# Kernel tuning notes

Measured on AMD Instinct MI355X. Metric: run time of the kernel, lower is better.

## Reference

```python
import jax, jax.numpy as jnp
import numpy as np

WIN = 7          # window height/width
P = 10           # prompts_len
HEADS = 12
B0 = 32          # image batch (spa_prompts batch)
NW = 64          # windows per image
NW_TOK = WIN * WIN  # 49


def _relative_position_index(w):
    coords = np.stack(np.meshgrid(np.arange(w), np.arange(w), indexing='ij'))  # [2,w,w]
    flat = coords.reshape(2, -1)                        # [2, w*w]
    rel = flat[:, :, None] - flat[:, None, :]           # [2, w*w, w*w]
    rel = rel.transpose(1, 2, 0).astype(np.int64)       # [w*w, w*w, 2]
    rel[..., 0] += w - 1
    rel[..., 1] += w - 1
    rel[..., 0] *= 2 * w - 1
    return rel.sum(-1)                                  # [w*w, w*w]

REL_IDX = jnp.asarray(_relative_position_index(WIN))    # [49,49] int


def setup_inputs() -> dict:
    key = jax.random.key(0)
    ks = jax.random.split(key, 8)
    dim = 384
    return {
        'x': jax.random.normal(ks[0], (B0 * NW, NW_TOK, dim), jnp.float32),
        'spa_prompts': jax.random.normal(ks[1], (B0, P, dim), jnp.float32),
        'mask': jax.random.normal(ks[2], (NW, NW_TOK, NW_TOK), jnp.float32),
        'bias_table': jax.random.normal(ks[3], (169, HEADS), jnp.float32) * 0.02,
        'w_qkv': jax.random.normal(ks[4], (3 * dim, dim), jnp.float32) * 0.02,
        'b_qkv': jax.random.normal(ks[5], (3 * dim,), jnp.float32) * 0.02,
        'w_proj': jax.random.normal(ks[6], (dim, dim), jnp.float32) * 0.02,
        'b_proj': jax.random.normal(ks[7], (dim,), jnp.float32) * 0.02,
    }


def reference(x, spa_prompts, mask, bias_table, w_qkv, b_qkv, w_proj, b_proj):
    B_, Nw, C = x.shape
    b0 = spa_prompts.shape[0]
    nW = B_ // b0
    hd = C // HEADS
    scale = hd ** -0.5

    # broadcast prompts to every window and prepend
    prompts = jnp.broadcast_to(spa_prompts[:, None], (b0, nW, P, C)).reshape(B_, P, C)
    xc = jnp.concatenate([prompts, x], axis=1)          # [B_, N, C], N = P + Nw
    N = xc.shape[1]

    qkv = xc @ w_qkv.T + b_qkv                          # [B_, N, 3C]
    qkv = qkv.reshape(B_, N, 3, HEADS, hd).transpose(2, 0, 3, 1, 4)
    q, k, v = qkv[0], qkv[1], qkv[2]                    # [B_, H, N, hd]

    attn_weight = jnp.einsum('bhnd,bhmd->bhnm', q, k)   # unscaled, returned

    # relative position bias gathered for the window block, padded over prompt rows/cols
    rpb = bias_table[REL_IDX.reshape(-1)].reshape(NW_TOK, NW_TOK, HEADS)
    rpb = rpb.transpose(2, 0, 1)                        # [H, 49, 49]
    bias_full = jnp.pad(rpb, ((0, 0), (P, 0), (P, 0)))  # [H, N, N]

    attn = attn_weight * scale + bias_full[None]

    mask_full = jnp.pad(mask, ((0, 0), (P, 0), (P, 0)))  # [nW, N, N]
    attn = attn.reshape(b0, nW, HEADS, N, N) + mask_full[None, :, None]
    attn = jax.nn.softmax(attn.reshape(B_, HEADS, N, N), axis=-1)

    out = jnp.einsum('bhnm,bhmd->bnhd', attn, v).reshape(B_, N, C)
    out = out @ w_proj.T + b_proj

    prompts_out = out[:, :P].reshape(b0, nW, P, C).mean(axis=1)
    x_out = out[:, P:]
    return (x_out, attn_weight, prompts_out)
```

## Files before the change

### kernel.cpp

```cpp
#include <hip/hip_runtime.h>
#include <hip/hip_bf16.h>

#define P     10
#define NTOK  59
#define HEADS 12
#define NWTOK 49

#define AW_OFF 38535168
#define PO_OFF 124096512

typedef __attribute__((ext_vector_type(8))) short short8;
typedef __attribute__((ext_vector_type(8))) unsigned short ushort8;
typedef __attribute__((ext_vector_type(4))) float floatx4;
typedef float f4u __attribute__((ext_vector_type(4), aligned(4)));
typedef unsigned int uint_g __attribute__((address_space(1)));
typedef unsigned int uint_l __attribute__((address_space(3)));

__device__ __forceinline__ unsigned short f2b(float f) {
  unsigned u = __builtin_bit_cast(unsigned, f);
  u += 0x7fffu + ((u >> 16) & 1u);
  return (unsigned short)(u >> 16);
}

__device__ __forceinline__ void gll16(const void* g, void* l) {
  __builtin_amdgcn_global_load_lds((const uint_g*)g, (uint_l*)l, 16, 0, 0);
}

__device__ __forceinline__ int xcd_swz(int bid, int nwg) {
  const int q = nwg >> 3, r = nwg & 7;
  const int xcd = bid & 7, ord = bid >> 3;
  return (xcd < r ? xcd * (q + 1) : r * (q + 1) + (xcd - r) * q) + ord;
}

__global__ __launch_bounds__(256) void convert_w_kernel(
    const float* __restrict__ w, unsigned short* __restrict__ wb) {
  const int i = (blockIdx.x * 256 + threadIdx.x) * 8;
  const float4 a = *(const float4*)(w + i);
  const float4 b = *(const float4*)(w + i + 4);
  ushort8 o;
  o[0] = f2b(a.x); o[1] = f2b(a.y); o[2] = f2b(a.z); o[3] = f2b(a.w);
  o[4] = f2b(b.x); o[5] = f2b(b.y); o[6] = f2b(b.z); o[7] = f2b(b.w);
  *(ushort8*)(wb + i) = o;
}

__global__ __launch_bounds__(256) void combo_kernel(
    const float* __restrict__ mask, const float* __restrict__ bias_table,
    float* __restrict__ combo) {
  const int bid = blockIdx.x;
  const int h = bid % HEADS, wnd = bid / HEADS;
#pragma unroll
  for (int e0 = 0; e0 < 4096; e0 += 256) {
    const int e = e0 + threadIdx.x;
    const int ti = e >> 6, tj = e & 63;
    float v = 0.f;
    if (ti >= P && ti < NTOK && tj >= P && tj < NTOK) {
      const int a = ti - P, c = tj - P;
      const int ai = a / 7, aj = a - ai * 7;
      const int bi = c / 7, bj = c - bi * 7;
      const int ridx = (ai - bi + 6) * 13 + (aj - bj + 6);
      v = bias_table[ridx * HEADS + h] + mask[((size_t)wnd * 49 + a) * 49 + c];
    }
    combo[((size_t)bid << 12) + e] = v;
  }
}

__global__ __launch_bounds__(256) void gemm_qkv_kernel(
    const unsigned short* __restrict__ xb, const unsigned short* __restrict__ xp,
    const unsigned short* __restrict__ Bw, const float* __restrict__ b_qkv,
    unsigned short* __restrict__ qkx, unsigned short* __restrict__ qkp) {
  __shared__ unsigned short sbuf[18432];
  unsigned short* Asw = sbuf;
  unsigned short* Bsw = sbuf + 8192;
  const int t = threadIdx.x;
  const int w = t >> 6, lane = t & 63;
  const int lr = lane & 15, lg = lane >> 4;
  const int w0 = w >> 1, w1 = w & 1;
  const int wg = xcd_swz(blockIdx.x, 9 * 787);
  const int cb = wg % 9;
  const int my = wg / 9;
  const bool isP = my >= 784;
  const int n0 = cb * 128;
  const int srow = lane >> 3, cpos = lane & 7;

  floatx4 acc[4][4];
#pragma unroll
  for (int mr = 0; mr < 4; ++mr)
#pragma unroll
    for (int nc = 0; nc < 4; ++nc) acc[mr][nc] = (floatx4)0.f;

  for (int k0 = 0; k0 < 384; k0 += 64) {
#pragma unroll
    for (int i = 0; i < 4; ++i) {
      const int r = (w * 4 + i) * 8 + srow;
      const int c = cpos ^ (r & 7);
      const unsigned short* asrc;
      if (!isP) {
        asrc = xb + (size_t)(my * 128 + r) * 384 + k0 + c * 8;
      } else {
        int mp = (my - 784) * 128 + r;
        if (mp > 319) mp = 319;
        asrc = xp + (size_t)mp * 384 + k0 + c * 8;
      }
      gll16(asrc, Asw + (w * 4 + i) * 512);
      gll16(Bw + (size_t)(n0 + r) * 384 + k0 + c * 8, Bsw + (w * 4 + i) * 512);
    }
    __syncthreads();
#pragma unroll
    for (int kh = 0; kh < 2; ++kh) {
      short8 af[4], bf[4];
#pragma unroll
      for (int mr = 0; mr < 4; ++mr) {
        const int r = w0 * 64 + mr * 16 + lr;
        af[mr] = *(const short8*)(Asw + r * 64 + (((kh * 4 + lg) ^ (r & 7)) * 8));
      }
#pragma unroll
      for (int nc = 0; nc < 4; ++nc) {
        const int r = w1 * 64 + nc * 16 + lr;
        bf[nc] = *(const short8*)(Bsw + r * 64 + (((kh * 4 + lg) ^ (r & 7)) * 8));
      }
#pragma unroll
      for (int mr = 0; mr < 4; ++mr)
#pragma unroll
        for (int nc = 0; nc < 4; ++nc)
          acc[mr][nc] = __builtin_amdgcn_mfma_f32_16x16x32_bf16(
              af[mr], bf[nc], acc[mr][nc], 0, 0, 0);
    }
    __syncthreads();
  }

  const int sec = cb / 3;
  const int nis = (cb - sec * 3) * 128;
  float bias[4];
#pragma unroll
  for (int nc = 0; nc < 4; ++nc)
    bias[nc] = b_qkv[n0 + w1 * 64 + nc * 16 + lr];

  unsigned short* rp = sbuf + w * 4608;
#pragma unroll
  for (int mr = 0; mr < 4; ++mr)
#pragma unroll
    for (int nc = 0; nc < 4; ++nc)
#pragma unroll
      for (int reg = 0; reg < 4; ++reg)
        rp[(mr * 16 + lg * 4 + reg) * 72 + nc * 16 + lr] =
            f2b(acc[mr][nc][reg] + bias[nc]);
  __syncthreads();

  const int rr = lane;
  unsigned short* dst = nullptr;
  if (!isP) {
    const int m = my * 128 + w0 * 64 + rr;
    const int bb = m / 49, tok = m - bb * 49;
    dst = qkx + ((size_t)(bb * 3 + sec) * 49 + tok) * 384 + nis + w1 * 64;
  } else {
    const int mp = (my - 784) * 128 + w0 * 64 + rr;
    if (mp < 320) {
      const int b0 = mp / 10, ptok = mp - b0 * 10;
      dst = qkp + ((size_t)(b0 * 3 + sec) * 10 + ptok) * 384 + nis + w1 * 64;
    }
  }
  if (dst) {
#pragma unroll
    for (int u = 0; u < 8; ++u)
      *(ushort8*)(dst + u * 8) = *(const ushort8*)(rp + rr * 72 + u * 8);
  }
}

__global__ __launch_bounds__(256) void attn_proj_kernel(
    const unsigned short* __restrict__ qkx, const unsigned short* __restrict__ qkp,
    const float* __restrict__ combo, const unsigned short* __restrict__ wproj,
    const float* __restrict__ b_proj, float* __restrict__ aw_out,
    float* __restrict__ x_out, float* __restrict__ pbuf) {
  __shared__ char lds[74752];
  unsigned short* Obuf = (unsigned short*)lds;
  unsigned short* qs   = (unsigned short*)(lds + 50176);
  unsigned short* ks   = (unsigned short*)(lds + 55296);
  unsigned short* vt   = (unsigned short*)(lds + 60416);
  unsigned short* Bst  = (unsigned short*)(lds + 50176);

  const int b = blockIdx.x;
  const int t = threadIdx.x;
  const int w = t >> 6, lane = t & 63, lr = lane & 15, lg = lane >> 4;
  const float scale = 0.17677669529663687f;
  const int q = w * 16 + lr;

  ushort8 nq, nk, nv;
  const int srow_ = t >> 2, sdc = (t & 3) * 8;
  auto load_head = [&](int h) {
    if (t < 236) {
      if (srow_ < P) {
        const unsigned short* pb =
            qkp + ((size_t)((b >> 6) * 3) * 10 + srow_) * 384 + h * 32 + sdc;
        nq = *(const ushort8*)(pb);
        nk = *(const ushort8*)(pb + 10 * 384);
        nv = *(const ushort8*)(pb + 20 * 384);
      } else {
        const unsigned short* xbp =
            qkx + ((size_t)(b * 3) * 49 + (srow_ - P)) * 384 + h * 32 + sdc;
        nq = *(const ushort8*)(xbp);
        nk = *(const ushort8*)(xbp + 49 * 384);
        nv = *(const ushort8*)(xbp + 98 * 384);
      }
    }
  };

  if (t < 160) vt[(t / 5) * 74 + 59 + (t % 5)] = 0;
  load_head(0);

  for (int h = 0; h < HEADS; ++h) {
    __syncthreads();
    if (t < 236) {
      *(ushort8*)(qs + srow_ * 40 + sdc) = nq;
      *(ushort8*)(ks + srow_ * 40 + sdc) = nk;
#pragma unroll
      for (int j = 0; j < 8; ++j) vt[(sdc + j) * 74 + srow_] = nv[j];
    }
    if (h + 1 < HEADS) load_head(h + 1);
    __syncthreads();

    const short8 qa = *(const short8*)(qs + q * 40 + lg * 8);
    floatx4 sacc[4];
#pragma unroll
    for (int nt = 0; nt < 4; ++nt) {
      const short8 kb = *(const short8*)(ks + (nt * 16 + lr) * 40 + lg * 8);
      sacc[nt] =
          __builtin_amdgcn_mfma_f32_16x16x32_bf16(kb, qa, (floatx4)0.f, 0, 0, 0);
    }

    if (q < NTOK) {
      float* rowp = aw_out + ((size_t)(b * HEADS + h)) * 3481 + q * 59;
#pragma unroll
      for (int nt = 0; nt < 3; ++nt)
        *(f4u*)(rowp + nt * 16 + lg * 4) = __builtin_bit_cast(f4u, sacc[nt]);
      if (lg < 2) {
        *(f4u*)(rowp + 48 + lg * 4) = __builtin_bit_cast(f4u, sacc[3]);
      } else if (lg == 2) {
        rowp[56] = sacc[3][0]; rowp[57] = sacc[3][1]; rowp[58] = sacc[3][2];
      }
    }

    const float* comb =
        combo + (((size_t)((b & 63) * HEADS + h)) << 12) + q * 64;
    float ev[4][4];
    float mx = -3.0e38f;
#pragma unroll
    for (int nt = 0; nt < 4; ++nt) {
      const float4 c4 = *(const float4*)(comb + nt * 16 + lg * 4);
      const float cc[4] = {c4.x, c4.y, c4.z, c4.w};
#pragma unroll
      for (int reg = 0; reg < 4; ++reg) {
        const int kk2 = nt * 16 + lg * 4 + reg;
        const float v = (q < NTOK && kk2 < NTOK)
                            ? fmaf(sacc[nt][reg], scale, cc[reg])
                            : -3.0e38f;
        ev[nt][reg] = v;
        mx = fmaxf(mx, v);
      }
    }
    mx = fmaxf(mx, __shfl_xor(mx, 16));
    mx = fmaxf(mx, __shfl_xor(mx, 32));
    float sm = 0.f;
#pragma unroll
    for (int nt = 0; nt < 4; ++nt)
#pragma unroll
      for (int reg = 0; reg < 4; ++reg) {
        const float e = __expf(ev[nt][reg] - mx);
        ev[nt][reg] = e;
        sm += e;
      }
    sm += __shfl_xor(sm, 16);
    sm += __shfl_xor(sm, 32);
    const float inv = 1.0f / sm;

    unsigned pk[4][2];
#pragma unroll
    for (int nt = 0; nt < 4; ++nt)
#pragma unroll
      for (int pp = 0; pp < 2; ++pp)
        pk[nt][pp] = (unsigned)f2b(ev[nt][2 * pp] * inv) |
                     ((unsigned)f2b(ev[nt][2 * pp + 1] * inv) << 16);

    floatx4 oacc[2];
    oacc[0] = (floatx4)0.f; oacc[1] = (floatx4)0.f;
#pragma unroll
    for (int kk = 0; kk < 2; ++kk) {
      unsigned W4[4];
#pragma unroll
      for (int jp = 0; jp < 4; ++jp) {
        const int srcl = lr + 16 * (2 * (lg & 1) + (jp >> 1));
        const int lo = __shfl((int)pk[2 * kk][jp & 1], srcl);
        const int hi = __shfl((int)pk[2 * kk + 1][jp & 1], srcl);
        W4[jp] = (lg >> 1) ? (unsigned)hi : (unsigned)lo;
      }
      uint4 wu; wu.x = W4[0]; wu.y = W4[1]; wu.z = W4[2]; wu.w = W4[3];
      const short8 pa = __builtin_bit_cast(short8, wu);
#pragma unroll
      for (int nt = 0; nt < 2; ++nt) {
        const short8 vb =
            *(const short8*)(vt + (nt * 16 + lr) * 74 + kk * 32 + lg * 8);
        oacc[nt] =
            __builtin_amdgcn_mfma_f32_16x16x32_bf16(pa, vb, oacc[nt], 0, 0, 0);
      }
    }

#pragma unroll
    for (int nt = 0; nt < 2; ++nt)
#pragma unroll
      for (int reg = 0; reg < 4; ++reg)
        Obuf[(w * 16 + lg * 4 + reg) * 392 + h * 32 + nt * 16 + lr] =
            f2b(oacc[nt][reg]);
  }

  ushort8 bst[6];
  auto load_proj = [&](int s) {
    const int nh_ = s / 6, kch_ = s % 6;
#pragma unroll
    for (int i = 0; i < 6; ++i) {
      const int g = w * 6 + i;
      const int r = g * 8 + (lane >> 3);
      const int c = (lane & 7) ^ (r & 7);
      bst[i] = *(const ushort8*)(wproj + (size_t)(nh_ * 192 + r) * 384 +
                                 kch_ * 64 + c * 8);
    }
  };
  load_proj(0);

  floatx4 pacc[12];
#pragma unroll
  for (int nh = 0; nh < 2; ++nh) {
#pragma unroll
    for (int i = 0; i < 12; ++i) pacc[i] = (floatx4)0.f;
    for (int kch = 0; kch < 6; ++kch) {
      const int s = nh * 6 + kch;
      __syncthreads();
#pragma unroll
      for (int i = 0; i < 6; ++i)
        *(ushort8*)(Bst + (size_t)(w * 6 + i) * 512 + lane * 8) = bst[i];
      if (s + 1 < 12) load_proj(s + 1);
      __syncthreads();
#pragma unroll
      for (int kh = 0; kh < 2; ++kh) {
        const short8 af = *(const short8*)(Obuf + (w * 16 + lr) * 392 +
                                           kch * 64 + kh * 32 + lg * 8);
#pragma unroll
        for (int nc = 0; nc < 12; ++nc) {
          const int nr = nc * 16 + lr;
          const short8 bf =
              *(const short8*)(Bst + nr * 64 + (((kh * 4 + lg) ^ (nr & 7)) * 8));
          pacc[nc] =
              __builtin_amdgcn_mfma_f32_16x16x32_bf16(af, bf, pacc[nc], 0, 0, 0);
        }
      }
    }
#pragma unroll
    for (int nc = 0; nc < 12; ++nc) {
      const int n = nh * 192 + nc * 16 + lr;
      const float bias = b_proj[n];
#pragma unroll
      for (int reg = 0; reg < 4; ++reg) {
        const int row = w * 16 + lg * 4 + reg;
        if (row < NTOK) {
          float* dst = (row >= P)
              ? x_out + ((size_t)(b * NWTOK + row - P)) * 384 + n
              : pbuf + ((size_t)(b * P + row)) * 384 + n;
          *dst = pacc[nc][reg] + bias;
        }
      }
    }
  }
}

__global__ __launch_bounds__(256) void reduce_prompts_kernel(
    const float* __restrict__ pbuf, float* __restrict__ po) {
  const int o = blockIdx.x * 256 + threadIdx.x;
  const int b0 = o / 3840;
  const int rem = o - b0 * 3840;
  const float* base = pbuf + (size_t)b0 * 64 * 3840 + rem;
  float s = 0.f;
#pragma unroll 8
  for (int w = 0; w < 64; ++w) s += base[(size_t)w * 3840];
  po[o] = s * (1.f / 64.f);
}

extern "C" void kernel_launch(void* const* d_in, const int* in_sizes, int n_in,
                              void* d_out, int out_size, void* d_ws, size_t ws_size,
                              hipStream_t stream) {
  const float* x          = (const float*)d_in[0];
  const float* spa        = (const float*)d_in[1];
  const float* mask       = (const float*)d_in[2];
  const float* bias_table = (const float*)d_in[3];
  const float* w_qkv      = (const float*)d_in[4];
  const float* b_qkv      = (const float*)d_in[5];
  const float* w_proj     = (const float*)d_in[6];
  const float* b_proj     = (const float*)d_in[7];
  float* out = (float*)d_out;

  unsigned short* x_bf     = (unsigned short*)d_ws;
  unsigned short* xp_bf    = (unsigned short*)((char*)d_ws + 77070336ULL);
  unsigned short* wqkv_bf  = (unsigned short*)((char*)d_ws + 77316096ULL);
  unsigned short* qkx      = (unsigned short*)((char*)d_ws + 92798976ULL);
  unsigned short* qkp      = (unsigned short*)((char*)d_ws + 324009984ULL);
  unsigned short* wproj_bf = (unsigned short*)((char*)d_ws + 324747264ULL);
  float*          pbuf     = (float*)((char*)d_ws + 325042176ULL);
  float*          combo    = (float*)((char*)d_ws + 356499456ULL);

  convert_w_kernel<<<18816, 256, 0, stream>>>(x, x_bf);
  convert_w_kernel<<<60, 256, 0, stream>>>(spa, xp_bf);
  convert_w_kernel<<<216, 256, 0, stream>>>(w_qkv, wqkv_bf);
  convert_w_kernel<<<72, 256, 0, stream>>>(w_proj, wproj_bf);
  combo_kernel<<<768, 256, 0, stream>>>(mask, bias_table, combo);
  gemm_qkv_kernel<<<9 * 787, 256, 0, stream>>>(x_bf, xp_bf, wqkv_bf, b_qkv,
                                               qkx, qkp);
  attn_proj_kernel<<<2048, 256, 0, stream>>>(qkx, qkp, combo, wproj_bf, b_proj,
                                             out + AW_OFF, out, pbuf);
  reduce_prompts_kernel<<<480, 256, 0, stream>>>(pbuf, out + PO_OFF);
}
```

Measured before the change: 586.9 us.

## Fuse per-head output projection into attention loop and split blocks by output half

The attention kernel now accumulates the output projection per head directly from the PV result held in registers, so the 50KB LDS buffer for the full attention output is no longer needed. Each window is handled by two blocks, each computing one half of the projection columns, which doubles the grid and recomputes attention in both blocks. Only one of the two writes the attention weights. LDS drops to about 25KB and launch bounds request 4 blocks per CU to raise occupancy. Q/K and projection weights are loaded with direct global-to-LDS loads into XOR-swizzled layouts, and blocks are remapped across XCDs for locality. The cost is the duplicated QK and softmax work.

```diff
diff --git a/kernel.cpp b/kernel.cpp
--- a/kernel.cpp
+++ b/kernel.cpp
@@ -166,68 +166,91 @@
   }
 }
 
-__global__ __launch_bounds__(256) void attn_proj_kernel(
+__global__ __launch_bounds__(256, 4) void attn_proj_kernel(
     const unsigned short* __restrict__ qkx, const unsigned short* __restrict__ qkp,
     const float* __restrict__ combo, const unsigned short* __restrict__ wproj,
     const float* __restrict__ b_proj, float* __restrict__ aw_out,
     float* __restrict__ x_out, float* __restrict__ pbuf) {
-  __shared__ char lds[74752];
-  unsigned short* Obuf = (unsigned short*)lds;
-  unsigned short* qs   = (unsigned short*)(lds + 50176);
-  unsigned short* ks   = (unsigned short*)(lds + 55296);
-  unsigned short* vt   = (unsigned short*)(lds + 60416);
-  unsigned short* Bst  = (unsigned short*)(lds + 50176);
-
-  const int b = blockIdx.x;
+  __shared__ char lds[25216];
+  unsigned short* qs = (unsigned short*)(lds);
+  unsigned short* ks = (unsigned short*)(lds + 4096);
+  unsigned short* vt = (unsigned short*)(lds + 8192);
+  unsigned short* wB = (unsigned short*)(lds + 12928);
+
+  const int bid = blockIdx.x;
+  const int xcd = bid & 7, idx = bid >> 3;
+  const int b = xcd * 256 + (idx >> 1);
+  const int half = idx & 1;
   const int t = threadIdx.x;
   const int w = t >> 6, lane = t & 63, lr = lane & 15, lg = lane >> 4;
   const float scale = 0.17677669529663687f;
   const int q = w * 16 + lr;
 
-  ushort8 nq, nk, nv;
+  const int gr = w * 16 + (lane >> 2);
+  const int gcl = (lane & 3) ^ (gr & 3);
+
+  ushort8 nv;
   const int srow_ = t >> 2, sdc = (t & 3) * 8;
-  auto load_head = [&](int h) {
+  auto load_v = [&](int h) {
     if (t < 236) {
-      if (srow_ < P) {
-        const unsigned short* pb =
-            qkp + ((size_t)((b >> 6) * 3) * 10 + srow_) * 384 + h * 32 + sdc;
-        nq = *(const ushort8*)(pb);
-        nk = *(const ushort8*)(pb + 10 * 384);
-        nv = *(const ushort8*)(pb + 20 * 384);
-      } else {
-        const unsigned short* xbp =
-            qkx + ((size_t)(b * 3) * 49 + (srow_ - P)) * 384 + h * 32 + sdc;
-        nq = *(const ushort8*)(xbp);
-        nk = *(const ushort8*)(xbp + 49 * 384);
-        nv = *(const ushort8*)(xbp + 98 * 384);
-      }
+      if (srow_ < P)
+        nv = *(const ushort8*)(qkp +
+            ((size_t)((b >> 6) * 3 + 2) * 10 + srow_) * 384 + h * 32 + sdc);
+      else
+        nv = *(const ushort8*)(qkx +
+            ((size_t)(b * 3 + 2) * 49 + (srow_ - P)) * 384 + h * 32 + sdc);
     }
   };
 
   if (t < 160) vt[(t / 5) * 74 + 59 + (t % 5)] = 0;
-  load_head(0);
+  load_v(0);
+
+  floatx4 pacc[12];
+#pragma unroll
+  for (int nc = 0; nc < 12; ++nc) pacc[nc] = (floatx4)0.f;
 
   for (int h = 0; h < HEADS; ++h) {
     __syncthreads();
     if (t < 236) {
-      *(ushort8*)(qs + srow_ * 40 + sdc) = nq;
-      *(ushort8*)(ks + srow_ * 40 + sdc) = nk;
 #pragma unroll
       for (int j = 0; j < 8; ++j) vt[(sdc + j) * 74 + srow_] = nv[j];
     }
-    if (h + 1 < HEADS) load_head(h + 1);
+    {
+      const unsigned short *qsrc, *ksrc;
+      if (gr < P) {
+        const size_t pb = ((size_t)((b >> 6) * 3) * 10 + gr) * 384 + h * 32 + gcl * 8;
+        qsrc = qkp + pb;
+        ksrc = qkp + pb + 10 * 384;
+      } else {
+        const size_t xb_ = ((size_t)(b * 3) * 49 + (gr - P)) * 384 + h * 32 + gcl * 8;
+        qsrc = qkx + xb_;
+        ksrc = qkx + xb_ + 49 * 384;
+      }
+      gll16(qsrc, qs + w * 512);
+      gll16(ksrc, ks + w * 512);
+    }
+#pragma unroll
+    for (int i = 0; i < 3; ++i) {
+      const int g = i * 4 + w;
+      const int r = g * 16 + (lane >> 2);
+      const int c = (lane & 3) ^ (r & 3);
+      gll16(wproj + (size_t)(half * 192 + r) * 384 + h * 32 + c * 8,
+            wB + g * 512);
+    }
+    if (h + 1 < HEADS) load_v(h + 1);
     __syncthreads();
 
-    const short8 qa = *(const short8*)(qs + q * 40 + lg * 8);
+    const short8 qa = *(const short8*)(qs + q * 32 + ((lg ^ (q & 3)) * 8));
     floatx4 sacc[4];
 #pragma unroll
     for (int nt = 0; nt < 4; ++nt) {
-      const short8 kb = *(const short8*)(ks + (nt * 16 + lr) * 40 + lg * 8);
+      const int r = nt * 16 + lr;
+      const short8 kb = *(const short8*)(ks + r * 32 + ((lg ^ (r & 3)) * 8));
       sacc[nt] =
           __builtin_amdgcn_mfma_f32_16x16x32_bf16(kb, qa, (floatx4)0.f, 0, 0, 0);
     }
 
-    if (q < NTOK) {
+    if (half == 0 && q < NTOK) {
       float* rowp = aw_out + ((size_t)(b * HEADS + h)) * 3481 + q * 59;
 #pragma unroll
       for (int nt = 0; nt < 3; ++nt)
@@ -241,7 +264,6 @@
 
     const float* comb =
         combo + (((size_t)((b & 63) * HEADS + h)) << 12) + q * 64;
-    float ev[4][4];
     float mx = -3.0e38f;
 #pragma unroll
     for (int nt = 0; nt < 4; ++nt) {
@@ -253,7 +275,7 @@
         const float v = (q < NTOK && kk2 < NTOK)
                             ? fmaf(sacc[nt][reg], scale, cc[reg])
                             : -3.0e38f;
-        ev[nt][reg] = v;
+        sacc[nt][reg] = v;
         mx = fmaxf(mx, v);
       }
     }
@@ -264,8 +286,8 @@
     for (int nt = 0; nt < 4; ++nt)
 #pragma unroll
       for (int reg = 0; reg < 4; ++reg) {
-        const float e = __expf(ev[nt][reg] - mx);
-        ev[nt][reg] = e;
+        const float e = __expf(sacc[nt][reg] - mx);
+        sacc[nt][reg] = e;
         sm += e;
       }
     sm += __shfl_xor(sm, 16);
@@ -277,11 +299,11 @@
     for (int nt = 0; nt < 4; ++nt)
 #pragma unroll
       for (int pp = 0; pp < 2; ++pp)
-        pk[nt][pp] = (unsigned)f2b(ev[nt][2 * pp] * inv) |
-                     ((unsigned)f2b(ev[nt][2 * pp + 1] * inv) << 16);
-
-    floatx4 oacc[2];
-    oacc[0] = (floatx4)0.f; oacc[1] = (floatx4)0.f;
+        pk[nt][pp] = (unsigned)f2b(sacc[nt][2 * pp] * inv) |
+                     ((unsigned)f2b(sacc[nt][2 * pp + 1] * inv) << 16);
+
+    floatx4 oaccT[2];
+    oaccT[0] = (floatx4)0.f; oaccT[1] = (floatx4)0.f;
 #pragma unroll
     for (int kk = 0; kk < 2; ++kk) {
       unsigned W4[4];
@@ -298,73 +320,50 @@
       for (int nt = 0; nt < 2; ++nt) {
         const short8 vb =
             *(const short8*)(vt + (nt * 16 + lr) * 74 + kk * 32 + lg * 8);
-        oacc[nt] =
-            __builtin_amdgcn_mfma_f32_16x16x32_bf16(pa, vb, oacc[nt], 0, 0, 0);
-      }
-    }
-
+        oaccT[nt] =
+            __builtin_amdgcn_mfma_f32_16x16x32_bf16(vb, pa, oaccT[nt], 0, 0, 0);
+      }
+    }
+
+    unsigned pko[2][2];
 #pragma unroll
     for (int nt = 0; nt < 2; ++nt)
 #pragma unroll
-      for (int reg = 0; reg < 4; ++reg)
-        Obuf[(w * 16 + lg * 4 + reg) * 392 + h * 32 + nt * 16 + lr] =
-            f2b(oacc[nt][reg]);
-  }
-
-  ushort8 bst[6];
-  auto load_proj = [&](int s) {
-    const int nh_ = s / 6, kch_ = s % 6;
-#pragma unroll
-    for (int i = 0; i < 6; ++i) {
-      const int g = w * 6 + i;
-      const int r = g * 8 + (lane >> 3);
-      const int c = (lane & 7) ^ (r & 7);
-      bst[i] = *(const ushort8*)(wproj + (size_t)(nh_ * 192 + r) * 384 +
-                                 kch_ * 64 + c * 8);
-    }
-  };
-  load_proj(0);
-
-  floatx4 pacc[12];
-#pragma unroll
-  for (int nh = 0; nh < 2; ++nh) {
-#pragma unroll
-    for (int i = 0; i < 12; ++i) pacc[i] = (floatx4)0.f;
-    for (int kch = 0; kch < 6; ++kch) {
-      const int s = nh * 6 + kch;
-      __syncthreads();
-#pragma unroll
-      for (int i = 0; i < 6; ++i)
-        *(ushort8*)(Bst + (size_t)(w * 6 + i) * 512 + lane * 8) = bst[i];
-      if (s + 1 < 12) load_proj(s + 1);
-      __syncthreads();
-#pragma unroll
-      for (int kh = 0; kh < 2; ++kh) {
-        const short8 af = *(const short8*)(Obuf + (w * 16 + lr) * 392 +
-                                           kch * 64 + kh * 32 + lg * 8);
-#pragma unroll
-        for (int nc = 0; nc < 12; ++nc) {
-          const int nr = nc * 16 + lr;
-          const short8 bf =
-              *(const short8*)(Bst + nr * 64 + (((kh * 4 + lg) ^ (nr & 7)) * 8));
-          pacc[nc] =
-              __builtin_amdgcn_mfma_f32_16x16x32_bf16(af, bf, pacc[nc], 0, 0, 0);
-        }
-      }
-    }
+      for (int pp = 0; pp < 2; ++pp)
+        pko[nt][pp] = (unsigned)f2b(oaccT[nt][2 * pp]) |
+                      ((unsigned)f2b(oaccT[nt][2 * pp + 1]) << 16);
+    unsigned W4[4];
+#pragma unroll
+    for (int jp = 0; jp < 4; ++jp) {
+      const int srcl = lr + 16 * (2 * (lg & 1) + (jp >> 1));
+      const int lo = __shfl((int)pko[0][jp & 1], srcl);
+      const int hi = __shfl((int)pko[1][jp & 1], srcl);
+      W4[jp] = (lg >> 1) ? (unsigned)hi : (unsigned)lo;
+    }
+    uint4 wu; wu.x = W4[0]; wu.y = W4[1]; wu.z = W4[2]; wu.w = W4[3];
+    const short8 af_o = __builtin_bit_cast(short8, wu);
+
 #pragma unroll
     for (int nc = 0; nc < 12; ++nc) {
-      const int n = nh * 192 + nc * 16 + lr;
-      const float bias = b_proj[n];
-#pragma unroll
-      for (int reg = 0; reg < 4; ++reg) {
-        const int row = w * 16 + lg * 4 + reg;
-        if (row < NTOK) {
-          float* dst = (row >= P)
-              ? x_out + ((size_t)(b * NWTOK + row - P)) * 384 + n
-              : pbuf + ((size_t)(b * P + row)) * 384 + n;
-          *dst = pacc[nc][reg] + bias;
-        }
+      const int r = nc * 16 + lr;
+      const short8 bfw = *(const short8*)(wB + r * 32 + ((lg ^ (r & 3)) * 8));
+      pacc[nc] =
+          __builtin_amdgcn_mfma_f32_16x16x32_bf16(af_o, bfw, pacc[nc], 0, 0, 0);
+    }
+  }
+
+#pragma unroll
+  for (int nc = 0; nc < 12; ++nc) {
+    const int n = half * 192 + nc * 16 + lr;
+    const float bias = b_proj[n];
+#pragma unroll
+    for (int reg = 0; reg < 4; ++reg) {
+      const int row = w * 16 + lg * 4 + reg;
+      if (row < NTOK) {
+        float* dst = (row >= P)
+            ? x_out + ((size_t)(b * NWTOK + row - P)) * 384 + n
+            : pbuf + ((size_t)(b * P + row)) * 384 + n;
+        *dst = pacc[nc][reg] + bias;
       }
     }
   }
@@ -411,7 +410,7 @@
   combo_kernel<<<768, 256, 0, stream>>>(mask, bias_table, combo);
   gemm_qkv_kernel<<<9 * 787, 256, 0, stream>>>(x_bf, xp_bf, wqkv_bf, b_qkv,
                                                qkx, qkp);
-  attn_proj_kernel<<<2048, 256, 0, stream>>>(qkx, qkp, combo, wproj_bf, b_proj,
+  attn_proj_kernel<<<4096, 256, 0, stream>>>(qkx, qkp, combo, wproj_bf, b_proj,
                                              out + AW_OFF, out, pbuf);
   reduce_prompts_kernel<<<480, 256, 0, stream>>>(pbuf, out + PO_OFF);
 }
```

Result: slower. 701.5 us (+19.5%).
